# Kernel tuning notes

Measured on AMD Instinct MI355X. Metric: run time of the kernel, lower is better.

The kernel has to match this reference:

```python
import jax, jax.numpy as jnp
import numpy as np

TEMPERATURE = 0.1
WEIGHT = 5.0
IS_SYMMETRIC = True


def setup_inputs() -> dict:
    key = jax.random.key(0)
    k1, k2, k3, k4, k5 = jax.random.split(key, 5)
    B, D = 2048, 128
    z_hat = jax.random.normal(k1, (1, B, D), dtype=jnp.float32)  # unused except batch size
    mu_x = jax.random.normal(k2, (B, D), dtype=jnp.float32)
    sigma_x = jax.random.uniform(k3, (B, D), minval=0.5, maxval=1.5, dtype=jnp.float32)
    mu_p = jax.random.normal(k4, (B, D), dtype=jnp.float32)
    sigma_p = jax.random.uniform(k5, (B, D), minval=0.5, maxval=1.5, dtype=jnp.float32)
    return {"z_hat": z_hat, "mu_x": mu_x, "sigma_x": sigma_x, "mu_p": mu_p, "sigma_p": sigma_p}


def _pairwise_kl(mus, sigmas):
    # K[a, b] = KL( N(mu_b, sig_b) || N(mu_a, sig_a) )  (matches torch repeat/repeat_interleave layout)
    D = mus.shape[1]
    var = sigmas * sigmas                      # [N, D]
    inv = 1.0 / var                            # [N, D]
    logdet = jnp.sum(jnp.log(sigmas), axis=1)  # [N]
    tr = jnp.einsum("ad,bd->ab", inv, var)                       # sum_d var_b / var_a
    quad = (jnp.einsum("ad,bd->ab", inv, mus * mus)
            - 2.0 * jnp.einsum("ad,bd->ab", mus * inv, mus)
            + jnp.sum(mus * mus * inv, axis=1)[:, None])         # sum_d (mu_b - mu_a)^2 / var_a
    return logdet[:, None] - logdet[None, :] + 0.5 * (tr + quad) - 0.5 * D


def reference(z_hat, mu_x, sigma_x, mu_p, sigma_p):
    B = mu_x.shape[0]
    N = 2 * B
    mus = jnp.concatenate([mu_x, mu_p], axis=0)       # [N, D]
    sigmas = jnp.concatenate([sigma_x, sigma_p], axis=0)

    logits = -_pairwise_kl(mus, sigmas)               # [N, N]
    if IS_SYMMETRIC:
        logits = (logits + logits.T) / 2
    logits = logits / TEMPERATURE

    # is_invariant=True: drop the diagonal -> [N, N-1] (static gather, jit-friendly)
    rows = jnp.arange(N)[:, None]
    cols = jnp.arange(N - 1)[None, :]
    idx = cols + (cols >= rows).astype(cols.dtype)    # skip column == row
    logits = jnp.take_along_axis(logits, jnp.broadcast_to(idx, (N, N - 1)), axis=1)

    n_classes = N - 1
    ar = jnp.arange(B)
    pos_idx = jnp.concatenate([ar + B - 1, ar], axis=0)  # [N]

    # weight != 1 branch: add -log(to_mult) at the positive logit of each row
    to_mult = (n_classes - 1.0 / WEIGHT) / (n_classes - 1)
    to_add = -jnp.log(jnp.asarray(to_mult, logits.dtype))
    logits = logits.at[jnp.arange(N), pos_idx].add(to_add)

    logp = jax.nn.log_softmax(logits, axis=1)
    hat_H_mlz = -jnp.mean(logp[jnp.arange(N), pos_idx])
    return hat_H_mlz
```

## Files before the change

kernel.cpp:

```cpp
#include <hip/hip_runtime.h>
#include <hip/hip_bf16.h>
#include <math.h>

typedef short bf16x8 __attribute__((ext_vector_type(8)));
typedef float f32x4 __attribute__((ext_vector_type(4)));

#define B_HALF 2048
#define N_TOT  4096
#define D_DIM  128
#define K_DIM  512
#define NGRP   32
#define NBLK   528
#define KSTEPS 16

__device__ unsigned red_done;

__global__ __launch_bounds__(256) void prep_feat(
    const float* __restrict__ mu_x, const float* __restrict__ sigma_x,
    const float* __restrict__ mu_p, const float* __restrict__ sigma_p,
    __hip_bfloat16* __restrict__ Gf, float* __restrict__ a) {
  const int tid = threadIdx.x;
  const int wv = tid >> 6;
  const int ln = tid & 63;
  const int d0 = ln * 2;
  const float SQ2 = 1.41421356237309515f;
#pragma unroll
  for (int rr = 0; rr < 16; rr += 4) {
    const int row = blockIdx.x * 16 + rr + wv;
    const float* mup = (row < B_HALF) ? mu_x : mu_p;
    const float* sgp = (row < B_HALF) ? sigma_x : sigma_p;
    const int gi = row & (B_HALF - 1);
    const float2 m2 = *(const float2*)(mup + gi * D_DIM + d0);
    const float2 s2 = *(const float2*)(sgp + gi * D_DIM + d0);
    float var0 = s2.x * s2.x, inv0 = 1.0f / var0, vm0 = var0 + m2.x * m2.x;
    float var1 = s2.y * s2.y, inv1 = 1.0f / var1, vm1 = var1 + m2.y * m2.y;
    size_t base = (size_t)row * K_DIM;
    __hip_bfloat162 h;
#define PK2(OFF, X, Y)                                                        \
    h.x = __float2bfloat16(X); h.y = __float2bfloat16(Y);                     \
    *(__hip_bfloat162*)(Gf + base + (OFF) + d0) = h;
    PK2(0,   inv0, inv1)
    PK2(128, vm0, vm1)
    PK2(256, SQ2 * m2.x * inv0, SQ2 * m2.y * inv1)
    PK2(384, -SQ2 * m2.x, -SQ2 * m2.y)
#undef PK2
    float av = m2.x * m2.x * inv0 + m2.y * m2.y * inv1;
#pragma unroll
    for (int x = 1; x < 64; x <<= 1) av += __shfl_xor(av, x);
    if (ln == 0) a[row] = av;
  }
}

#define GLOAD16(src, dst)                                                     \
  __builtin_amdgcn_global_load_lds(                                           \
      (const __attribute__((address_space(1))) void*)(src),                   \
      (__attribute__((address_space(3))) void*)(dst), 16, 0, 0)

__global__ __launch_bounds__(256, 3) void gemm_lse(
    const __hip_bfloat16* __restrict__ Gf, const float* __restrict__ a,
    float* __restrict__ lsep, float* __restrict__ pos, float to_add) {
  __shared__ char lt[3][128 * 64];
  __shared__ char rt[3][128 * 64];
  __shared__ float2 red[128][2];

  const int sb = (blockIdx.x & 7) * (NBLK / 8) + (blockIdx.x >> 3);
  int t = sb, rb = 0;
  while (t >= 32 - rb) { t -= 32 - rb; ++rb; }
  const int cb = rb + t;

  const int tid  = threadIdx.x;
  const int lane = tid & 63;
  const int wave = tid >> 6;
  const int rowBase = rb * 128, colBase = cb * 128;
  const int wr = wave >> 1, wc = wave & 1;
  const int lx = lane & 15;
  const int rq = lane >> 4;

  f32x4 acc[4][4];
#pragma unroll
  for (int m = 0; m < 4; ++m)
#pragma unroll
    for (int n = 0; n < 4; ++n) acc[m][n] = (f32x4){0.f, 0.f, 0.f, 0.f};

  const int sr  = lane >> 2;
  const int scb = (((lane & 3) ^ (sr & 3)) << 4);
  const char* lsrc0 = (const char*)Gf + (size_t)rowBase * (K_DIM * 2);
  const char* rsrc0 = (const char*)Gf + (size_t)colBase * (K_DIM * 2);

#define STAGE(KK)                                                             \
  {                                                                           \
    const int b_ = (KK) % 3;                                                  \
    const char* ls_ = lsrc0 + (KK) * 64;                                      \
    const char* rs_ = rsrc0 + ((KK) ^ 4) * 64;                                \
    _Pragma("unroll")                                                         \
    for (int g = 0; g < 2; ++g) {                                             \
      const int row_ = wave * 32 + g * 16;                                    \
      GLOAD16(ls_ + (size_t)(row_ + sr) * 1024 + scb, &lt[b_][row_ * 64]);    \
      GLOAD16(rs_ + (size_t)(row_ + sr) * 1024 + scb, &rt[b_][row_ * 64]);    \
    }                                                                         \
  }

  STAGE(0)
  STAGE(1)

#pragma unroll
  for (int kk = 0; kk < KSTEPS; ++kk) {
    if (kk < KSTEPS - 1) asm volatile("s_waitcnt vmcnt(4)" ::: "memory");
    else                 asm volatile("s_waitcnt vmcnt(0)" ::: "memory");
    __builtin_amdgcn_s_barrier();
    __builtin_amdgcn_sched_barrier(0);
    if (kk + 2 < KSTEPS) STAGE(kk + 2)
    const int b = kk % 3;
    bf16x8 af[4], bg[4];
    const int kbp = ((rq ^ (lx & 3)) << 4);
#pragma unroll
    for (int m = 0; m < 4; ++m) {
      const int row = wr * 64 + m * 16 + lx;
      af[m] = *(const bf16x8*)(&lt[b][row * 64 + kbp]);
    }
#pragma unroll
    for (int n = 0; n < 4; ++n) {
      const int row = wc * 64 + n * 16 + lx;
      bg[n] = *(const bf16x8*)(&rt[b][row * 64 + kbp]);
    }
#pragma unroll
    for (int m = 0; m < 4; ++m)
#pragma unroll
      for (int n = 0; n < 4; ++n)
        acc[m][n] = __builtin_amdgcn_mfma_f32_16x16x32_bf16(af[m], bg[n], acc[m][n], 0, 0, 0);
  }
#undef STAGE

  const float c0 = 640.0f;
  const float c1 = 2.5f;
  float aR[4][4];
#pragma unroll
  for (int m = 0; m < 4; ++m)
#pragma unroll
    for (int v = 0; v < 4; ++v)
      aR[m][v] = a[rowBase + wr * 64 + m * 16 + rq * 4 + v];
  float aC[4];
#pragma unroll
  for (int n = 0; n < 4; ++n) aC[n] = a[colBase + wc * 64 + n * 16 + lx];

#pragma unroll
  for (int m = 0; m < 4; ++m)
#pragma unroll
    for (int n = 0; n < 4; ++n)
#pragma unroll
      for (int v = 0; v < 4; ++v) {
        int grow = rowBase + wr * 64 + m * 16 + rq * 4 + v;
        int gcol = colBase + wc * 64 + n * 16 + lx;
        float S = c0 - c1 * (acc[m][n][v] + aR[m][v] + aC[n]);
        if (gcol == grow) {
          S = -INFINITY;
        } else if (gcol == (grow ^ B_HALF)) {
          S += to_add;
          pos[grow] = S;
          pos[gcol] = S;
        }
        acc[m][n][v] = S;
      }

#pragma unroll
  for (int m = 0; m < 4; ++m)
#pragma unroll
    for (int v = 0; v < 4; ++v) {
      float pm = -INFINITY;
#pragma unroll
      for (int n = 0; n < 4; ++n) pm = fmaxf(pm, acc[m][n][v]);
#pragma unroll
      for (int x = 1; x < 16; x <<= 1) pm = fmaxf(pm, __shfl_xor(pm, x));
      float ps = 0.f;
#pragma unroll
      for (int n = 0; n < 4; ++n) ps += __expf(acc[m][n][v] - pm);
#pragma unroll
      for (int x = 1; x < 16; x <<= 1) ps += __shfl_xor(ps, x);
      if (lx == 0) red[wr * 64 + m * 16 + rq * 4 + v][wc] = make_float2(pm, ps);
    }
  __syncthreads();
  if (tid < 128) {
    float2 p0 = red[tid][0], p1 = red[tid][1];
    float M = fmaxf(p0.x, p1.x);
    float S = p0.y * __expf(p0.x - M) + p1.y * __expf(p1.x - M);
    lsep[(size_t)(rowBase + tid) * NGRP + cb] = M + logf(S);
  }

  if (rb != cb) {
    __syncthreads();
#pragma unroll
    for (int n = 0; n < 4; ++n) {
      float cm = -INFINITY;
#pragma unroll
      for (int m = 0; m < 4; ++m)
#pragma unroll
        for (int v = 0; v < 4; ++v) cm = fmaxf(cm, acc[m][n][v]);
      cm = fmaxf(cm, __shfl_xor(cm, 16));
      cm = fmaxf(cm, __shfl_xor(cm, 32));
      float cs = 0.f;
#pragma unroll
      for (int m = 0; m < 4; ++m)
#pragma unroll
        for (int v = 0; v < 4; ++v) cs += __expf(acc[m][n][v] - cm);
      cs += __shfl_xor(cs, 16);
      cs += __shfl_xor(cs, 32);
      if (lane < 16) red[wc * 64 + n * 16 + lane][wr] = make_float2(cm, cs);
    }
    __syncthreads();
    if (tid < 128) {
      float2 p0 = red[tid][0], p1 = red[tid][1];
      float M = fmaxf(p0.x, p1.x);
      float S = p0.y * __expf(p0.x - M) + p1.y * __expf(p1.x - M);
      lsep[(size_t)(colBase + tid) * NGRP + rb] = M + logf(S);
    }
  }
}

__global__ __launch_bounds__(256) void reduce_final(
    const float* __restrict__ lsep, const float* __restrict__ pos,
    float* __restrict__ partial, float* __restrict__ out) {
  const int tid = threadIdx.x;
  const int row = blockIdx.x * 256 + tid;
  const float* lp = lsep + (size_t)row * NGRP;
  float M = lp[0];
#pragma unroll
  for (int k = 1; k < NGRP; ++k) M = fmaxf(M, lp[k]);
  float s = 0.f;
#pragma unroll
  for (int k = 0; k < NGRP; ++k) s += __expf(lp[k] - M);
  float contrib = (M + logf(s)) - pos[row];

  __shared__ float fr[256];
  fr[tid] = contrib;
  __syncthreads();
#pragma unroll
  for (int off = 128; off > 0; off >>= 1) {
    if (tid < off) fr[tid] += fr[tid + off];
    __syncthreads();
  }
  if (tid == 0) {
    partial[blockIdx.x] = fr[0];
    unsigned v = __hip_atomic_fetch_add(&red_done, 1u, __ATOMIC_ACQ_REL,
                                        __HIP_MEMORY_SCOPE_AGENT);
    if (v == 15u) {
      float tot = 0.f;
      for (int k = 0; k < 16; ++k) tot += partial[k];
      out[0] = tot * (1.0f / 4096.0f);
      __hip_atomic_store(&red_done, 0u, __ATOMIC_RELAXED,
                         __HIP_MEMORY_SCOPE_AGENT);
    }
  }
}

extern "C" void kernel_launch(void* const* d_in, const int* in_sizes, int n_in,
                              void* d_out, int out_size, void* d_ws, size_t ws_size,
                              hipStream_t stream) {
  const float* mu_x    = (const float*)d_in[1];
  const float* sigma_x = (const float*)d_in[2];
  const float* mu_p    = (const float*)d_in[3];
  const float* sigma_p = (const float*)d_in[4];
  float* out = (float*)d_out;

  float to_add = (float)(-log((4095.0 - 1.0 / 5.0) / 4094.0));

  const size_t featB = (size_t)N_TOT * K_DIM * 2;
  char* ws = (char*)d_ws;
  __hip_bfloat16* Gf = (__hip_bfloat16*)(ws);
  float* a       = (float*)(ws + featB);
  float* lsep    = (float*)(ws + featB + 16384);
  float* pos     = (float*)(ws + featB + 16384 + 524288);
  float* partial = (float*)(ws + featB + 16384 + 524288 + 16384);

  prep_feat<<<dim3(256), dim3(256), 0, stream>>>(mu_x, sigma_x, mu_p, sigma_p,
                                                 Gf, a);
  gemm_lse<<<dim3(NBLK), dim3(256), 0, stream>>>(Gf, a, lsep, pos, to_add);
  reduce_final<<<dim3(16), dim3(256), 0, stream>>>(lsep, pos, partial, out);
}
```

Before: 40.74 us.

## Enlarge GEMM tiles to 256x256 with 512-thread blocks and double buffering

The symmetric GEMM+log-sum-exp kernel moves from 128x128 tiles (528 upper-triangle blocks, 256 threads, triple-buffered 64-byte K slices) to 256x256 tiles (136 blocks, 512 threads, double-buffered 128-byte K slices with an XOR swizzle). Partial LSE groups per row drop from 32 to 16, which shrinks the lsep buffer and the final reduction work. The goal is more data reuse per block and fewer partial results. The cost is that 136 large blocks using 128 KB of LDS each cannot fill all CUs, and each K step gains an extra barrier. Feature stores in the prep kernel also become nontemporal.

```diff
diff --git a/kernel.cpp b/kernel.cpp
--- a/kernel.cpp
+++ b/kernel.cpp
@@ -9,9 +9,8 @@
 #define N_TOT  4096
 #define D_DIM  128
 #define K_DIM  512
-#define NGRP   32
-#define NBLK   528
-#define KSTEPS 16
+#define NGRP   16
+#define NBLK   136
 
 __device__ unsigned red_done;
 
@@ -36,9 +35,11 @@
     float var1 = s2.y * s2.y, inv1 = 1.0f / var1, vm1 = var1 + m2.y * m2.y;
     size_t base = (size_t)row * K_DIM;
     __hip_bfloat162 h;
+    unsigned ub;
 #define PK2(OFF, X, Y)                                                        \
     h.x = __float2bfloat16(X); h.y = __float2bfloat16(Y);                     \
-    *(__hip_bfloat162*)(Gf + base + (OFF) + d0) = h;
+    __builtin_memcpy(&ub, &h, 4);                                             \
+    __builtin_nontemporal_store(ub, (unsigned*)(Gf + base + (OFF) + d0));
     PK2(0,   inv0, inv1)
     PK2(128, vm0, vm1)
     PK2(256, SQ2 * m2.x * inv0, SQ2 * m2.y * inv1)
@@ -47,7 +48,7 @@
     float av = m2.x * m2.x * inv0 + m2.y * m2.y * inv1;
 #pragma unroll
     for (int x = 1; x < 64; x <<= 1) av += __shfl_xor(av, x);
-    if (ln == 0) a[row] = av;
+    if (ln == 0) __builtin_nontemporal_store(av, &a[row]);
   }
 }
 
@@ -56,47 +57,46 @@
       (const __attribute__((address_space(1))) void*)(src),                   \
       (__attribute__((address_space(3))) void*)(dst), 16, 0, 0)
 
-__global__ __launch_bounds__(256, 3) void gemm_lse(
+__global__ __launch_bounds__(512, 2) void gemm_lse(
     const __hip_bfloat16* __restrict__ Gf, const float* __restrict__ a,
     float* __restrict__ lsep, float* __restrict__ pos, float to_add) {
-  __shared__ char lt[3][128 * 64];
-  __shared__ char rt[3][128 * 64];
-  __shared__ float2 red[128][2];
+  __shared__ char smem[2][65536];
 
   const int sb = (blockIdx.x & 7) * (NBLK / 8) + (blockIdx.x >> 3);
   int t = sb, rb = 0;
-  while (t >= 32 - rb) { t -= 32 - rb; ++rb; }
+  while (t >= 16 - rb) { t -= 16 - rb; ++rb; }
   const int cb = rb + t;
 
   const int tid  = threadIdx.x;
   const int lane = tid & 63;
   const int wave = tid >> 6;
-  const int rowBase = rb * 128, colBase = cb * 128;
-  const int wr = wave >> 1, wc = wave & 1;
+  const int wr = wave >> 2;
+  const int wc = wave & 3;
   const int lx = lane & 15;
   const int rq = lane >> 4;
-
-  f32x4 acc[4][4];
-#pragma unroll
-  for (int m = 0; m < 4; ++m)
+  const int rowBase = rb * 256, colBase = cb * 256;
+
+  f32x4 acc[8][4];
+#pragma unroll
+  for (int m = 0; m < 8; ++m)
 #pragma unroll
     for (int n = 0; n < 4; ++n) acc[m][n] = (f32x4){0.f, 0.f, 0.f, 0.f};
 
-  const int sr  = lane >> 2;
-  const int scb = (((lane & 3) ^ (sr & 3)) << 4);
-  const char* lsrc0 = (const char*)Gf + (size_t)rowBase * (K_DIM * 2);
-  const char* rsrc0 = (const char*)Gf + (size_t)colBase * (K_DIM * 2);
+  const int srow = lane >> 3;
+  const char* gb = (const char*)Gf;
 
 #define STAGE(KK)                                                             \
   {                                                                           \
-    const int b_ = (KK) % 3;                                                  \
-    const char* ls_ = lsrc0 + (KK) * 64;                                      \
-    const char* rs_ = rsrc0 + ((KK) ^ 4) * 64;                                \
+    const int b_ = (KK) & 1;                                                  \
     _Pragma("unroll")                                                         \
-    for (int g = 0; g < 2; ++g) {                                             \
-      const int row_ = wave * 32 + g * 16;                                    \
-      GLOAD16(ls_ + (size_t)(row_ + sr) * 1024 + scb, &lt[b_][row_ * 64]);    \
-      GLOAD16(rs_ + (size_t)(row_ + sr) * 1024 + scb, &rt[b_][row_ * 64]);    \
+    for (int g = 0; g < 4; ++g) {                                             \
+      const int br   = wave * 32 + g * 8;                                     \
+      const int row_ = br + srow;                                             \
+      const int sq   = ((lane & 7) ^ (row_ & 7)) << 4;                        \
+      GLOAD16(gb + (size_t)(rowBase + row_) * 1024 + (KK) * 128 + sq,         \
+              &smem[b_][br * 128]);                                           \
+      GLOAD16(gb + (size_t)(colBase + row_) * 1024 + ((KK) ^ 2) * 128 + sq,   \
+              &smem[b_][32768 + br * 128]);                                   \
     }                                                                         \
   }
 
@@ -104,52 +104,59 @@
   STAGE(1)
 
 #pragma unroll
-  for (int kk = 0; kk < KSTEPS; ++kk) {
-    if (kk < KSTEPS - 1) asm volatile("s_waitcnt vmcnt(4)" ::: "memory");
-    else                 asm volatile("s_waitcnt vmcnt(0)" ::: "memory");
+  for (int kk = 0; kk < 8; ++kk) {
+    if (kk < 7) asm volatile("s_waitcnt vmcnt(8)" ::: "memory");
+    else        asm volatile("s_waitcnt vmcnt(0)" ::: "memory");
     __builtin_amdgcn_s_barrier();
     __builtin_amdgcn_sched_barrier(0);
-    if (kk + 2 < KSTEPS) STAGE(kk + 2)
-    const int b = kk % 3;
-    bf16x8 af[4], bg[4];
-    const int kbp = ((rq ^ (lx & 3)) << 4);
-#pragma unroll
-    for (int m = 0; m < 4; ++m) {
-      const int row = wr * 64 + m * 16 + lx;
-      af[m] = *(const bf16x8*)(&lt[b][row * 64 + kbp]);
-    }
-#pragma unroll
-    for (int n = 0; n < 4; ++n) {
-      const int row = wc * 64 + n * 16 + lx;
-      bg[n] = *(const bf16x8*)(&rt[b][row * 64 + kbp]);
-    }
-#pragma unroll
-    for (int m = 0; m < 4; ++m)
-#pragma unroll
-      for (int n = 0; n < 4; ++n)
-        acc[m][n] = __builtin_amdgcn_mfma_f32_16x16x32_bf16(af[m], bg[n], acc[m][n], 0, 0, 0);
+    const int b = kk & 1;
+#pragma unroll
+    for (int ks = 0; ks < 2; ++ks) {
+      bf16x8 af[8], bg[4];
+      const int lq = ks * 4 + rq;
+#pragma unroll
+      for (int m = 0; m < 8; ++m) {
+        const int row = wr * 128 + m * 16 + lx;
+        af[m] = *(const bf16x8*)&smem[b][row * 128 + ((lq ^ (row & 7)) << 4)];
+      }
+#pragma unroll
+      for (int n = 0; n < 4; ++n) {
+        const int row = wc * 64 + n * 16 + lx;
+        bg[n] = *(const bf16x8*)&smem[b][32768 + row * 128 + ((lq ^ (row & 7)) << 4)];
+      }
+#pragma unroll
+      for (int m = 0; m < 8; ++m)
+#pragma unroll
+        for (int n = 0; n < 4; ++n)
+          acc[m][n] = __builtin_amdgcn_mfma_f32_16x16x32_bf16(af[m], bg[n], acc[m][n], 0, 0, 0);
+    }
+    __builtin_amdgcn_s_barrier();
+    if (kk + 2 < 8) STAGE(kk + 2)
   }
 #undef STAGE
+
+  __syncthreads();
+  float2 (*red)[4] = (float2 (*)[4])&smem[0][0];
 
   const float c0 = 640.0f;
   const float c1 = 2.5f;
-  float aR[4][4];
-#pragma unroll
-  for (int m = 0; m < 4; ++m)
+  float aR[8][4];
+#pragma unroll
+  for (int m = 0; m < 8; ++m)
 #pragma unroll
     for (int v = 0; v < 4; ++v)
-      aR[m][v] = a[rowBase + wr * 64 + m * 16 + rq * 4 + v];
+      aR[m][v] = a[rowBase + wr * 128 + m * 16 + rq * 4 + v];
   float aC[4];
 #pragma unroll
   for (int n = 0; n < 4; ++n) aC[n] = a[colBase + wc * 64 + n * 16 + lx];
 
 #pragma unroll
-  for (int m = 0; m < 4; ++m)
+  for (int m = 0; m < 8; ++m)
 #pragma unroll
     for (int n = 0; n < 4; ++n)
 #pragma unroll
       for (int v = 0; v < 4; ++v) {
-        int grow = rowBase + wr * 64 + m * 16 + rq * 4 + v;
+        int grow = rowBase + wr * 128 + m * 16 + rq * 4 + v;
         int gcol = colBase + wc * 64 + n * 16 + lx;
         float S = c0 - c1 * (acc[m][n][v] + aR[m][v] + aC[n]);
         if (gcol == grow) {
@@ -163,7 +170,7 @@
       }
 
 #pragma unroll
-  for (int m = 0; m < 4; ++m)
+  for (int m = 0; m < 8; ++m)
 #pragma unroll
     for (int v = 0; v < 4; ++v) {
       float pm = -INFINITY;
@@ -176,13 +183,16 @@
       for (int n = 0; n < 4; ++n) ps += __expf(acc[m][n][v] - pm);
 #pragma unroll
       for (int x = 1; x < 16; x <<= 1) ps += __shfl_xor(ps, x);
-      if (lx == 0) red[wr * 64 + m * 16 + rq * 4 + v][wc] = make_float2(pm, ps);
+      if (lx == 0) red[wr * 128 + m * 16 + rq * 4 + v][wc] = make_float2(pm, ps);
     }
   __syncthreads();
-  if (tid < 128) {
-    float2 p0 = red[tid][0], p1 = red[tid][1];
-    float M = fmaxf(p0.x, p1.x);
-    float S = p0.y * __expf(p0.x - M) + p1.y * __expf(p1.x - M);
+  if (tid < 256) {
+    float M = -INFINITY;
+#pragma unroll
+    for (int g = 0; g < 4; ++g) M = fmaxf(M, red[tid][g].x);
+    float S = 0.f;
+#pragma unroll
+    for (int g = 0; g < 4; ++g) S += red[tid][g].y * __expf(red[tid][g].x - M);
     lsep[(size_t)(rowBase + tid) * NGRP + cb] = M + logf(S);
   }
 
@@ -192,14 +202,14 @@
     for (int n = 0; n < 4; ++n) {
       float cm = -INFINITY;
 #pragma unroll
-      for (int m = 0; m < 4; ++m)
+      for (int m = 0; m < 8; ++m)
 #pragma unroll
         for (int v = 0; v < 4; ++v) cm = fmaxf(cm, acc[m][n][v]);
       cm = fmaxf(cm, __shfl_xor(cm, 16));
       cm = fmaxf(cm, __shfl_xor(cm, 32));
       float cs = 0.f;
 #pragma unroll
-      for (int m = 0; m < 4; ++m)
+      for (int m = 0; m < 8; ++m)
 #pragma unroll
         for (int v = 0; v < 4; ++v) cs += __expf(acc[m][n][v] - cm);
       cs += __shfl_xor(cs, 16);
@@ -207,7 +217,7 @@
       if (lane < 16) red[wc * 64 + n * 16 + lane][wr] = make_float2(cm, cs);
     }
     __syncthreads();
-    if (tid < 128) {
+    if (tid < 256) {
       float2 p0 = red[tid][0], p1 = red[tid][1];
       float M = fmaxf(p0.x, p1.x);
       float S = p0.y * __expf(p0.x - M) + p1.y * __expf(p1.x - M);
@@ -266,13 +276,14 @@
   const size_t featB = (size_t)N_TOT * K_DIM * 2;
   char* ws = (char*)d_ws;
   __hip_bfloat16* Gf = (__hip_bfloat16*)(ws);
-  float* a       = (float*)(ws + featB);
-  float* lsep    = (float*)(ws + featB + 16384);
-  float* pos     = (float*)(ws + featB + 16384 + 524288);
-  float* partial = (float*)(ws + featB + 16384 + 524288 + 16384);
+  size_t off = featB;
+  float* a       = (float*)(ws + off); off += 16384;
+  float* lsep    = (float*)(ws + off); off += (size_t)N_TOT * NGRP * 4;
+  float* pos     = (float*)(ws + off); off += 16384;
+  float* partial = (float*)(ws + off); off += 16384;
 
   prep_feat<<<dim3(256), dim3(256), 0, stream>>>(mu_x, sigma_x, mu_p, sigma_p,
                                                  Gf, a);
-  gemm_lse<<<dim3(NBLK), dim3(256), 0, stream>>>(Gf, a, lsep, pos, to_add);
+  gemm_lse<<<dim3(NBLK), dim3(512), 0, stream>>>(Gf, a, lsep, pos, to_add);
   reduce_final<<<dim3(16), dim3(256), 0, stream>>>(lsep, pos, partial, out);
 }
```

Result: slower. 46.69 us (+14.6%).
